# Optimization experiments

Hardware: AMD Instinct MI355X
Metric: run time of the kernel (lower is better)

The kernel has to match this reference:

```python
import jax, jax.numpy as jnp
import numpy as np

B, T, R = 32, 200, 8192
TOPK_RATIO = 0.05
K = int(R * TOPK_RATIO)            # 409 selected regions
K2 = int(R * TOPK_RATIO ** 2)      # 20 compressed features
REST = R - K                        # 7783 == rest_limitation
BN_EPS = 1e-5
NORM_EPS = 1e-12


def _linear_params(key, fan_in, fan_out):
    kw, kb = jax.random.split(key)
    bound = 1.0 / np.sqrt(fan_in)
    w = jax.random.uniform(kw, (fan_out, fan_in), jnp.float32, -bound, bound)
    b = jax.random.uniform(kb, (fan_out,), jnp.float32, -bound, bound)
    return w, b


def setup_inputs() -> dict:
    key = jax.random.key(0)
    ks = jax.random.split(key, 8)
    x = jax.random.normal(ks[0], (B, T, R), jnp.float32)
    w_proj, b_proj = _linear_params(ks[1], T, 1)
    w_process, b_process = _linear_params(ks[2], K, K)
    w_compress, b_compress = _linear_params(ks[3], K, K2)
    w_unzip, b_unzip = _linear_params(ks[4], K2, K)
    w_unprocess, b_unprocess = _linear_params(ks[5], K, K)
    w_rest, b_rest = _linear_params(ks[6], K, REST)
    bn_gamma = jnp.ones((T,), jnp.float32)
    bn_beta = jnp.zeros((T,), jnp.float32)
    return {
        "x": x,
        "w_proj": w_proj[0], "b_proj": b_proj,
        "w_process": w_process, "b_process": b_process,
        "bn_gamma": bn_gamma, "bn_beta": bn_beta,
        "w_compress": w_compress, "b_compress": b_compress,
        "w_unzip": w_unzip, "b_unzip": b_unzip,
        "w_unprocess": w_unprocess, "b_unprocess": b_unprocess,
        "w_rest": w_rest, "b_rest": b_rest,
    }


def reference(x, w_proj, b_proj, w_process, b_process, bn_gamma, bn_beta,
              w_compress, b_compress, w_unzip, b_unzip,
              w_unprocess, b_unprocess, w_rest, b_rest):
    # ---------------- Encoder ----------------
    border_mask = jnp.isnan(x)                       # [B,T,R]
    x = jnp.where(border_mask, 0.0, x)
    # F.normalize over the time axis (dim=1)
    nrm = jnp.sqrt(jnp.sum(x * x, axis=1, keepdims=True))
    x = x / jnp.maximum(nrm, NORM_EPS)
    # projection: Linear(T,1) on x.transpose(-1,-2) -> score [B,R]
    score = jnp.einsum('btr,t->br', x, w_proj) + b_proj
    border_limit = jnp.mean(border_mask.astype(x.dtype), axis=1)   # [B,R]
    score = jnp.where(border_limit.astype(bool), -10000.0, score)
    _, index = jax.lax.top_k(score, K)               # [B,K] (descending score order)
    x_topk = jnp.take_along_axis(x, index[:, None, :], axis=2)  # [B,T,K]
    sel = jnp.zeros((B, R), x.dtype).at[jnp.arange(B)[:, None], index].set(1.0)
    mask = jnp.broadcast_to(sel[:, None, :], (B, T, R))
    # process: Linear(K,K) + BatchNorm1d(T) in training mode (batch stats)
    h = jnp.einsum('btk,jk->btj', x_topk, w_process) + b_process
    mu = jnp.mean(h, axis=(0, 2), keepdims=True)
    var = jnp.var(h, axis=(0, 2), keepdims=True)     # biased, as torch BN
    h = (h - mu) / jnp.sqrt(var + BN_EPS)
    h = h * bn_gamma[None, :, None] + bn_beta[None, :, None]
    x_compress = jnp.einsum('btk,jk->btj', h, w_compress) + b_compress  # [B,T,K2]

    # ---------------- Decoder ----------------
    z = jnp.einsum('btc,kc->btk', x_compress, w_unzip) + b_unzip
    z = jnp.einsum('btk,jk->btj', z, w_unprocess) + b_unprocess          # [B,T,K]
    z_rest = jnp.einsum('btk,rk->btr', z, w_rest) + b_rest               # [B,T,REST]
    # rest positions: columns neither NaN-bordered nor topk-selected, ascending
    occupied = jnp.logical_or(sel.astype(bool), jnp.any(border_mask, axis=1))  # [B,R]
    rest_pos = jax.vmap(lambda s: jnp.argsort(s)[:REST])(occupied)       # [B,REST]

    def scat(zv, zr, idx, rp):
        xr = jnp.zeros((T, R), zv.dtype)
        xr = xr.at[:, idx].set(zv)
        xr = xr.at[:, rp].set(zr)
        return xr

    x_recon = jax.vmap(scat)(z, z_rest, index, rest_pos)                 # [B,T,R]
    return (x_recon, x_compress, mask, border_mask, index)
```

## Files before the change

kernel.cpp:

```cpp
#include <hip/hip_runtime.h>

#define Bz 32
#define Tz 200
#define Rz 8192
#define Kz 409
#define KP 416
#define K2 20
#define K2P 32
#define RESTz 7783

typedef __bf16 bf16x8 __attribute__((ext_vector_type(8)));
typedef float f32x4 __attribute__((ext_vector_type(4)));

__launch_bounds__(256)
__global__ void k_padcast(const float* __restrict__ src, __bf16* __restrict__ dst,
                          int N, int Kd, int Npad, int Kpad) {
    int i = blockIdx.x * 256 + threadIdx.x;
    int total = Npad * Kpad;
    if (i >= total) return;
    int r = i / Kpad, c = i - r * Kpad;
    float v = (r < N && c < Kd) ? src[(size_t)r * Kd + c] : 0.f;
    dst[i] = (__bf16)v;
}

__launch_bounds__(256)
__global__ void k_stats(const float* __restrict__ x, const float* __restrict__ w_proj,
                        const float* __restrict__ b_proj,
                        float* __restrict__ invnrm, float* __restrict__ score,
                        int* __restrict__ bordany, float* __restrict__ border_out) {
    const int b = blockIdx.y;
    const int c = blockIdx.x * 256 + threadIdx.x;
    const float* xp = x + (size_t)b * Tz * Rz + c;
    float* bp = border_out + (size_t)b * Tz * Rz + c;
    float p[32];
#pragma unroll
    for (int y = 0; y < 32; ++y) p[y] = 0.f;
    int nn = 0;
    for (int k = 0; k < 7; ++k) {
        const int tbase = k * 32;
#pragma unroll
        for (int y = 0; y < 32; ++y) {
            const int t = tbase + y;
            if (t < Tz) {
                float v = xp[(size_t)t * Rz];
                bool isn = (v != v);
                nn |= isn ? 1 : 0;
                float val = isn ? 0.f : v;
                bp[(size_t)t * Rz] = isn ? 1.0f : 0.0f;
                p[y] = __fadd_rn(p[y], __fmul_rn(val, val));
            }
        }
    }
#pragma unroll
    for (int off = 16; off > 0; off >>= 1)
#pragma unroll
        for (int y = 0; y < 16; ++y)
            if (y < off) p[y] = __fadd_rn(p[y], p[y + off]);
    const float ss = p[0];
    const float nv = fmaxf(__fsqrt_rn(ss), 1e-12f);
    float q[32];
#pragma unroll
    for (int y = 0; y < 32; ++y) q[y] = 0.f;
    for (int k = 0; k < 7; ++k) {
        const int tbase = k * 32;
#pragma unroll
        for (int y = 0; y < 32; ++y) {
            const int t = tbase + y;
            if (t < Tz) {
                float v = xp[(size_t)t * Rz];
                float val = (v != v) ? 0.f : v;
                float xn = __fdiv_rn(val, nv);
                float e = __fmul_rn(xn, w_proj[t]);
                q[y] = __fadd_rn(q[y], e);
            }
        }
    }
#pragma unroll
    for (int off = 16; off > 0; off >>= 1)
#pragma unroll
        for (int y = 0; y < 16; ++y)
            if (y < off) q[y] = __fadd_rn(q[y], q[y + off]);
    float sc = __fadd_rn(q[0], b_proj[0]);
    if (nn) sc = -10000.f;
    invnrm[(size_t)b * Rz + c] = __fdiv_rn(1.0f, nv);
    score[(size_t)b * Rz + c] = sc;
    bordany[(size_t)b * Rz + c] = nn;
}

__launch_bounds__(1024)
__global__ void k_topk(const float* __restrict__ score, const int* __restrict__ bordany,
                       int* __restrict__ index_ws, int* __restrict__ rest_pos,
                       float* __restrict__ o_index) {
    const int b = blockIdx.x;
    const int tid = threadIdx.x;
    __shared__ unsigned su[Rz];
    __shared__ unsigned hist[256];
    __shared__ unsigned sfx[256];
    __shared__ unsigned ckey[512];
    __shared__ unsigned cidx[512];
    __shared__ unsigned cnum;
    __shared__ unsigned sh_prefix;
    __shared__ int sh_need;
    __shared__ int scnt[1024];

    for (int i = tid; i < Rz; i += 1024) {
        unsigned u = __float_as_uint(score[(size_t)b * Rz + i]);
        u = (u & 0x80000000u) ? ~u : (u | 0x80000000u);
        su[i] = u;
    }
    __syncthreads();

    unsigned prefix = 0u, pmask = 0u;
    int need = Kz;
    for (int byte = 3; byte >= 0; --byte) {
        const int sh = byte * 8;
        if (tid < 256) hist[tid] = 0u;
        __syncthreads();
        for (int i = tid; i < Rz; i += 1024) {
            unsigned u = su[i];
            if ((u & pmask) == prefix) atomicAdd(&hist[(u >> sh) & 255u], 1u);
        }
        __syncthreads();
        if (tid < 256) sfx[tid] = hist[tid];
        __syncthreads();
        for (int off = 1; off < 256; off <<= 1) {
            unsigned add = 0u;
            if (tid < 256 && tid + off < 256) add = sfx[tid + off];
            __syncthreads();
            if (tid < 256) sfx[tid] += add;
            __syncthreads();
        }
        if (tid < 256) {
            unsigned above = (tid == 255) ? 0u : sfx[tid + 1];
            if (sfx[tid] >= (unsigned)need && above < (unsigned)need) {
                sh_need = need - (int)above;
                sh_prefix = prefix | ((unsigned)tid << sh);
            }
        }
        __syncthreads();
        prefix = sh_prefix;
        need = sh_need;
        pmask |= (0xFFu << sh);
        __syncthreads();
    }
    const unsigned Tval = prefix;

    if (tid == 0) cnum = 0u;
    __syncthreads();
    for (int i = tid; i < Rz; i += 1024) {
        unsigned u = su[i];
        if (u >= Tval) {
            unsigned p = atomicAdd(&cnum, 1u);
            if (p < 512u) { ckey[p] = u; cidx[p] = (unsigned)i; }
        }
    }
    __syncthreads();
    const int cn = (cnum < 512u) ? (int)cnum : 512;
    for (int i = tid; i < 512; i += 1024)
        if (i >= cn) { ckey[i] = 0u; cidx[i] = 0xFFFFFFFFu; }
    __syncthreads();

    for (int kk = 2; kk <= 512; kk <<= 1) {
        for (int j = kk >> 1; j > 0; j >>= 1) {
            if (tid < 256) {
                const int i = ((tid & ~(j - 1)) << 1) | (tid & (j - 1));
                const int l = i | j;
                unsigned ka = ckey[i], kb = ckey[l];
                unsigned ia = cidx[i], ib = cidx[l];
                bool a_after_b = (ka < kb) || (ka == kb && ia > ib);
                bool b_after_a = (kb < ka) || (kb == ka && ib > ia);
                bool desc = ((i & kk) == 0);
                bool dosw = desc ? a_after_b : b_after_a;
                if (dosw) { ckey[i] = kb; ckey[l] = ka; cidx[i] = ib; cidx[l] = ia; }
            }
            __syncthreads();
        }
    }

    for (int i = tid; i < Kz; i += 1024) {
        int idx = (int)(cidx[i] & 8191u);
        index_ws[b * Kz + i] = idx;
        o_index[(size_t)b * Kz + i] = (float)idx;
    }
    __syncthreads();
    for (int i = tid; i < Rz; i += 1024)
        su[i] = (bordany[(size_t)b * Rz + i] != 0) ? 1u : 0u;
    __syncthreads();
    for (int i = tid; i < Kz; i += 1024) su[cidx[i] & 8191u] = 1u;
    __syncthreads();
    int cnt = 0;
    {
        const int base = tid * 8;
#pragma unroll
        for (int o = 0; o < 8; ++o) cnt += (su[base + o] == 0u) ? 1 : 0;
    }
    scnt[tid] = cnt;
    __syncthreads();
    for (int offp = 1; offp < 1024; offp <<= 1) {
        int add = (tid >= offp) ? scnt[tid - offp] : 0;
        __syncthreads();
        scnt[tid] += add;
        __syncthreads();
    }
    const int total_un = scnt[1023];
    int run = scnt[tid] - cnt;
    const int base = tid * 8;
    for (int o = 0; o < 8; ++o) {
        const int c = base + o;
        const bool un = (su[c] == 0u);
        int pos = un ? run : (total_un + (c - run));
        if (un) run++;
        if (pos < RESTz) rest_pos[b * RESTz + pos] = c;
    }
}

__launch_bounds__(256)
__global__ void k_gather(const float* __restrict__ x, const float* __restrict__ invnrm,
                         const int* __restrict__ index_ws, __bf16* __restrict__ x_topk) {
    const int m = blockIdx.x;
    const int b = m / Tz;
    const float* xrow = x + (size_t)m * Rz;
    for (int kk = threadIdx.x; kk < KP; kk += 256) {
        float val = 0.f;
        if (kk < Kz) {
            const unsigned idx = (unsigned)index_ws[b * Kz + kk] & 8191u;
            float v = xrow[idx];
            if (v != v) v = 0.f;
            val = __fmul_rn(v, invnrm[(size_t)b * Rz + idx]);
        }
        x_topk[(size_t)m * KP + kk] = (__bf16)val;
    }
}

__launch_bounds__(256)
__global__ void k_bn(const __bf16* __restrict__ h, const float* __restrict__ gamma,
                     const float* __restrict__ beta, __bf16* __restrict__ hbn) {
    const int t = blockIdx.x;
    const int tid = threadIdx.x;
    float s = 0.f, s2 = 0.f;
    for (int i = tid; i < Bz * Kz; i += 256) {
        int b = i / Kz, j = i - b * Kz;
        float v = (float)h[(size_t)(b * Tz + t) * KP + j];
        s += v;
        s2 += v * v;
    }
    for (int off = 32; off > 0; off >>= 1) {
        s += __shfl_down(s, off);
        s2 += __shfl_down(s2, off);
    }
    __shared__ float rs[4], rs2[4];
    __shared__ float sc_sh, sf_sh;
    const int wid = tid >> 6;
    if ((tid & 63) == 0) { rs[wid] = s; rs2[wid] = s2; }
    __syncthreads();
    if (tid == 0) {
        float S = rs[0] + rs[1] + rs[2] + rs[3];
        float S2 = rs2[0] + rs2[1] + rs2[2] + rs2[3];
        const float invN = 1.f / (float)(Bz * Kz);
        float mu = S * invN;
        float var = S2 * invN - mu * mu;
        float rstd = rsqrtf(var + 1e-5f);
        float scl = gamma[t] * rstd;
        sc_sh = scl;
        sf_sh = beta[t] - mu * scl;
    }
    __syncthreads();
    const float scl = sc_sh, sft = sf_sh;
    for (int i = tid; i < Bz * KP; i += 256) {
        int b = i / KP, j = i - b * KP;
        float outv = 0.f;
        if (j < Kz) {
            float v = (float)h[(size_t)(b * Tz + t) * KP + j];
            outv = v * scl + sft;
        }
        hbn[(size_t)(b * Tz + t) * KP + j] = (__bf16)outv;
    }
}

__launch_bounds__(256)
__global__ void k_mask(const int* __restrict__ index_ws, float* __restrict__ o_mask) {
    const int bt = blockIdx.x;
    const int b = bt / Tz;
    const int tid = threadIdx.x;
    __shared__ unsigned bm[256];
    bm[tid] = 0u;
    __syncthreads();
    for (int i = tid; i < Kz; i += 256) {
        unsigned idx = (unsigned)index_ws[b * Kz + i] & 8191u;
        atomicOr(&bm[idx >> 5], 1u << (idx & 31u));
    }
    __syncthreads();
    const unsigned bits = bm[tid];
    float* dst = o_mask + (size_t)bt * Rz + tid * 32;
#pragma unroll
    for (int g = 0; g < 8; ++g) {
        float4 v;
        v.x = ((bits >> (g * 4 + 0)) & 1u) ? 1.0f : 0.0f;
        v.y = ((bits >> (g * 4 + 1)) & 1u) ? 1.0f : 0.0f;
        v.z = ((bits >> (g * 4 + 2)) & 1u) ? 1.0f : 0.0f;
        v.w = ((bits >> (g * 4 + 3)) & 1u) ? 1.0f : 0.0f;
        *(float4*)(dst + g * 4) = v;
    }
}

template <int EPI>
__launch_bounds__(256)
__global__ void k_gemm(const __bf16* __restrict__ A, int lda, int ksteps,
                       const __bf16* __restrict__ Wb, int ldb,
                       const float* __restrict__ bias,
                       __bf16* __restrict__ b_out,
                       float* __restrict__ o_xc,
                       const int* __restrict__ index_ws,
                       const int* __restrict__ rest_pos,
                       float* __restrict__ o_recon) {
    __shared__ __bf16 As[128][32];
    __shared__ __bf16 Bs[128][32];
    const int m0 = blockIdx.x * 128;
    const int n0 = blockIdx.y * 128;
    const int tid = threadIdx.x;
    const int lane = tid & 63;
    const int wid = tid >> 6;
    const int wm = wid >> 1, wn = wid & 1;
    const int r0 = lane >> 2;
    const int sg = (lane & 3) * 8;
    const int fr = lane & 15;
    const int fg = lane >> 4;
    f32x4 acc[4][4];
#pragma unroll
    for (int i = 0; i < 4; ++i)
#pragma unroll
        for (int j = 0; j < 4; ++j) {
            f32x4 z = {0.f, 0.f, 0.f, 0.f};
            acc[i][j] = z;
        }

    const int ca = wid * 16 + r0;
    const int cb = (wid + 4) * 16 + r0;
    const __bf16* gA0 = A + (size_t)(m0 + ca) * lda + sg;
    const __bf16* gA1 = A + (size_t)(m0 + cb) * lda + sg;
    const __bf16* gB0 = Wb + (size_t)(n0 + ca) * ldb + sg;
    const __bf16* gB1 = Wb + (size_t)(n0 + cb) * ldb + sg;
    __bf16* lA0 = &As[wid * 16][0];
    __bf16* lA1 = &As[(wid + 4) * 16][0];
    __bf16* lB0 = &Bs[wid * 16][0];
    __bf16* lB1 = &Bs[(wid + 4) * 16][0];

    for (int s = 0; s < ksteps; ++s) {
        const int k0 = s * 32;
        __syncthreads();
        __builtin_amdgcn_global_load_lds(gA0 + k0, lA0, 16, 0, 0);
        __builtin_amdgcn_global_load_lds(gA1 + k0, lA1, 16, 0, 0);
        __builtin_amdgcn_global_load_lds(gB0 + k0, lB0, 16, 0, 0);
        __builtin_amdgcn_global_load_lds(gB1 + k0, lB1, 16, 0, 0);
        __syncthreads();
        bf16x8 af[4], bf[4];
#pragma unroll
        for (int mi = 0; mi < 4; ++mi)
            af[mi] = *(const bf16x8*)&As[wm * 64 + mi * 16 + fr][fg * 8];
#pragma unroll
        for (int ni = 0; ni < 4; ++ni)
            bf[ni] = *(const bf16x8*)&Bs[wn * 64 + ni * 16 + fr][fg * 8];
#pragma unroll
        for (int mi = 0; mi < 4; ++mi)
#pragma unroll
            for (int ni = 0; ni < 4; ++ni)
                acc[mi][ni] = __builtin_amdgcn_mfma_f32_16x16x32_bf16(af[mi], bf[ni],
                                                                      acc[mi][ni], 0, 0, 0);
    }

#pragma unroll
    for (int mi = 0; mi < 4; ++mi)
#pragma unroll
        for (int ni = 0; ni < 4; ++ni)
#pragma unroll
            for (int rr = 0; rr < 4; ++rr) {
                const int gm = m0 + wm * 64 + mi * 16 + fg * 4 + rr;
                const int gn = n0 + wn * 64 + ni * 16 + fr;
                const float v = acc[mi][ni][rr];
                if constexpr (EPI == 0) {
                    if (gn < KP) {
                        float val = (gn < Kz) ? (v + bias[gn]) : 0.f;
                        b_out[(size_t)gm * KP + gn] = (__bf16)val;
                    }
                } else if constexpr (EPI == 1) {
                    if (gn < K2P) {
                        float val = (gn < K2) ? (v + bias[gn]) : 0.f;
                        if (gn < K2) o_xc[(size_t)gm * K2 + gn] = val;
                        b_out[(size_t)gm * K2P + gn] = (__bf16)val;
                    }
                } else if constexpr (EPI == 2) {
                    if (gn < KP) {
                        float val = (gn < Kz) ? (v + bias[gn]) : 0.f;
                        b_out[(size_t)gm * KP + gn] = (__bf16)val;
                    }
                } else if constexpr (EPI == 3) {
                    if (gn < KP) {
                        float val = (gn < Kz) ? (v + bias[gn]) : 0.f;
                        b_out[(size_t)gm * KP + gn] = (__bf16)val;
                        if (gn < Kz) {
                            const int bb = gm / Tz;
                            const unsigned col = (unsigned)index_ws[bb * Kz + gn] & 8191u;
                            o_recon[(size_t)gm * Rz + col] = val;
                        }
                    }
                } else {
                    if (gn < RESTz) {
                        const float val = v + bias[gn];
                        const int bb = gm / Tz;
                        const unsigned col = (unsigned)rest_pos[bb * RESTz + gn] & 8191u;
                        o_recon[(size_t)gm * Rz + col] = val;
                    }
                }
            }
}

extern "C" void kernel_launch(void* const* d_in, const int* in_sizes, int n_in,
                              void* d_out, int out_size, void* d_ws, size_t ws_size,
                              hipStream_t stream) {
    (void)in_sizes; (void)n_in; (void)out_size;
    const float* x           = (const float*)d_in[0];
    const float* w_proj      = (const float*)d_in[1];
    const float* b_proj      = (const float*)d_in[2];
    const float* w_process   = (const float*)d_in[3];
    const float* b_process   = (const float*)d_in[4];
    const float* bn_gamma    = (const float*)d_in[5];
    const float* bn_beta     = (const float*)d_in[6];
    const float* w_compress  = (const float*)d_in[7];
    const float* b_compress  = (const float*)d_in[8];
    const float* w_unzip     = (const float*)d_in[9];
    const float* b_unzip     = (const float*)d_in[10];
    const float* w_unprocess = (const float*)d_in[11];
    const float* b_unprocess = (const float*)d_in[12];
    const float* w_rest      = (const float*)d_in[13];
    const float* b_rest      = (const float*)d_in[14];

    float* out = (float*)d_out;
    float* o_recon  = out;
    float* o_xc     = o_recon + (size_t)Bz * Tz * Rz;
    float* o_mask   = o_xc + (size_t)Bz * Tz * K2;
    float* o_border = o_mask + (size_t)Bz * Tz * Rz;
    float* o_index  = o_border + (size_t)Bz * Tz * Rz;

    const size_t SLOT = ((size_t)Bz * Tz * KP * 2 + 255) & ~(size_t)255;
    const size_t IDXB = ((size_t)Bz * Kz * 4 + 255) & ~(size_t)255;
    const size_t RESB = ((size_t)Bz * RESTz * 4 + 255) & ~(size_t)255;
    const size_t WPB  = ((size_t)512 * KP * 2 + 255) & ~(size_t)255;
    const size_t WZB  = ((size_t)512 * K2P * 2 + 255) & ~(size_t)255;
    const size_t WCB  = ((size_t)128 * KP * 2 + 255) & ~(size_t)255;
    const size_t need = 3 * SLOT + IDXB + RESB + 2 * WPB + WZB + WCB;
    if (ws_size < need) return;

    char* ws = (char*)d_ws;
    __bf16* S1 = (__bf16*)(ws);
    __bf16* S2 = (__bf16*)(ws + SLOT);
    __bf16* S3 = (__bf16*)(ws + 2 * SLOT);
    int* index_ws = (int*)(ws + 3 * SLOT);
    int* rest_pos = (int*)(ws + 3 * SLOT + IDXB);
    __bf16* wp_b  = (__bf16*)(ws + 3 * SLOT + IDXB + RESB);
    __bf16* wup_b = (__bf16*)(ws + 3 * SLOT + IDXB + RESB + WPB);
    __bf16* wz_b  = (__bf16*)(ws + 3 * SLOT + IDXB + RESB + 2 * WPB);
    __bf16* wc_b  = (__bf16*)(ws + 3 * SLOT + IDXB + RESB + 2 * WPB + WZB);
    __bf16* wrest_b = (__bf16*)(ws);

    float* invnrm = (float*)S2;
    float* score  = invnrm + (size_t)Bz * Rz;
    int*   bordany = (int*)(score + (size_t)Bz * Rz);

    __bf16* x_topk = S1;
    __bf16* hbuf   = S2;
    __bf16* hbn    = S3;
    __bf16* xc_pad = S2;
    __bf16* z1     = S1;
    __bf16* zb     = S3;

    auto PC = [&](const float* src, __bf16* dst, int N, int Kd, int Npad, int Kpad) {
        int total = Npad * Kpad;
        k_padcast<<<dim3((total + 255) / 256), dim3(256), 0, stream>>>(src, dst, N, Kd, Npad, Kpad);
    };
    PC(w_process, wp_b, Kz, Kz, 512, KP);
    PC(w_unprocess, wup_b, Kz, Kz, 512, KP);
    PC(w_unzip, wz_b, Kz, K2, 512, K2P);
    PC(w_compress, wc_b, K2, Kz, 128, KP);

    k_stats<<<dim3(Rz / 256, Bz), dim3(256), 0, stream>>>(x, w_proj, b_proj, invnrm, score,
                                                          bordany, o_border);
    k_topk<<<dim3(Bz), dim3(1024), 0, stream>>>(score, bordany, index_ws, rest_pos, o_index);
    k_gather<<<dim3(Bz * Tz), dim3(256), 0, stream>>>(x, invnrm, index_ws, x_topk);

    dim3 blk(256);
    k_gemm<0><<<dim3(50, 4), blk, 0, stream>>>(x_topk, KP, 13, wp_b, KP, b_process,
                                               hbuf, nullptr, nullptr, nullptr, nullptr);
    k_bn<<<dim3(Tz), blk, 0, stream>>>(hbuf, bn_gamma, bn_beta, hbn);
    k_gemm<1><<<dim3(50, 1), blk, 0, stream>>>(hbn, KP, 13, wc_b, KP, b_compress,
                                               xc_pad, o_xc, nullptr, nullptr, nullptr);
    k_gemm<2><<<dim3(50, 4), blk, 0, stream>>>(xc_pad, K2P, 1, wz_b, K2P, b_unzip,
                                               z1, nullptr, nullptr, nullptr, nullptr);
    k_gemm<3><<<dim3(50, 4), blk, 0, stream>>>(z1, KP, 13, wup_b, KP, b_unprocess,
                                               zb, nullptr, index_ws, nullptr, o_recon);
    PC(w_rest, wrest_b, RESTz, Kz, 7808, KP);
    k_gemm<4><<<dim3(50, 61), blk, 0, stream>>>(zb, KP, 13, wrest_b, KP, b_rest,
                                                nullptr, nullptr, nullptr, rest_pos, o_recon);
    k_mask<<<dim3(Bz * Tz), dim3(256), 0, stream>>>(index_ws, o_mask);
}
```

Before: 604.7 us.

## Fold decoder linear chain into composed weights applied to compressed features

```diff
diff --git a/kernel.cpp b/kernel.cpp
--- a/kernel.cpp
+++ b/kernel.cpp
@@ -21,6 +21,52 @@
     int r = i / Kpad, c = i - r * Kpad;
     float v = (r < N && c < Kd) ? src[(size_t)r * Kd + c] : 0.f;
     dst[i] = (__bf16)v;
+}
+
+__launch_bounds__(32)
+__global__ void k_wu(const float* __restrict__ wup, const float* __restrict__ wz,
+                     const float* __restrict__ b_uz, const float* __restrict__ b_up,
+                     float* __restrict__ WU_f, float* __restrict__ bU,
+                     __bf16* __restrict__ WU_b) {
+    const int i = blockIdx.x;
+    const int c = threadIdx.x;
+    if (i >= Kz) {
+        if (c < K2P) WU_b[(size_t)i * K2P + c] = (__bf16)0.f;
+        return;
+    }
+    const float* row = wup + (size_t)i * Kz;
+    float acc = 0.f;
+    if (c < K2) {
+        for (int j = 0; j < Kz; ++j) acc = fmaf(row[j], wz[(size_t)j * K2 + c], acc);
+        WU_f[(size_t)i * K2 + c] = acc;
+        WU_b[(size_t)i * K2P + c] = (__bf16)acc;
+    } else if (c == K2) {
+        for (int j = 0; j < Kz; ++j) acc = fmaf(row[j], b_uz[j], acc);
+        bU[i] = acc + b_up[i];
+    }
+    if (c >= K2 && c < K2P) WU_b[(size_t)i * K2P + c] = (__bf16)0.f;
+}
+
+__launch_bounds__(32)
+__global__ void k_wr(const float* __restrict__ wr, const float* __restrict__ b_r,
+                     const float* __restrict__ WU_f, const float* __restrict__ bU,
+                     __bf16* __restrict__ WR_b, float* __restrict__ bR) {
+    const int r = blockIdx.x;
+    const int c = threadIdx.x;
+    if (r >= RESTz) {
+        if (c < K2P) WR_b[(size_t)r * K2P + c] = (__bf16)0.f;
+        return;
+    }
+    const float* row = wr + (size_t)r * Kz;
+    float acc = 0.f;
+    if (c < K2) {
+        for (int i = 0; i < Kz; ++i) acc = fmaf(row[i], WU_f[(size_t)i * K2 + c], acc);
+        WR_b[(size_t)r * K2P + c] = (__bf16)acc;
+    } else if (c == K2) {
+        for (int i = 0; i < Kz; ++i) acc = fmaf(row[i], bU[i], acc);
+        bR[r] = acc + b_r[r];
+    }
+    if (c >= K2 && c < K2P) WR_b[(size_t)r * K2P + c] = (__bf16)0.f;
 }
 
 __launch_bounds__(256)
@@ -388,20 +434,12 @@
                         if (gn < K2) o_xc[(size_t)gm * K2 + gn] = val;
                         b_out[(size_t)gm * K2P + gn] = (__bf16)val;
                     }
-                } else if constexpr (EPI == 2) {
-                    if (gn < KP) {
-                        float val = (gn < Kz) ? (v + bias[gn]) : 0.f;
-                        b_out[(size_t)gm * KP + gn] = (__bf16)val;
-                    }
                 } else if constexpr (EPI == 3) {
-                    if (gn < KP) {
-                        float val = (gn < Kz) ? (v + bias[gn]) : 0.f;
-                        b_out[(size_t)gm * KP + gn] = (__bf16)val;
-                        if (gn < Kz) {
-                            const int bb = gm / Tz;
-                            const unsigned col = (unsigned)index_ws[bb * Kz + gn] & 8191u;
-                            o_recon[(size_t)gm * Rz + col] = val;
-                        }
+                    if (gn < Kz) {
+                        float val = v + bias[gn];
+                        const int bb = gm / Tz;
+                        const unsigned col = (unsigned)index_ws[bb * Kz + gn] & 8191u;
+                        o_recon[(size_t)gm * Rz + col] = val;
                     }
                 } else {
                     if (gn < RESTz) {
@@ -445,22 +483,30 @@
     const size_t IDXB = ((size_t)Bz * Kz * 4 + 255) & ~(size_t)255;
     const size_t RESB = ((size_t)Bz * RESTz * 4 + 255) & ~(size_t)255;
     const size_t WPB  = ((size_t)512 * KP * 2 + 255) & ~(size_t)255;
-    const size_t WZB  = ((size_t)512 * K2P * 2 + 255) & ~(size_t)255;
     const size_t WCB  = ((size_t)128 * KP * 2 + 255) & ~(size_t)255;
-    const size_t need = 3 * SLOT + IDXB + RESB + 2 * WPB + WZB + WCB;
+    const size_t WUF  = ((size_t)Kz * K2 * 4 + 255) & ~(size_t)255;
+    const size_t BUB  = ((size_t)512 * 4 + 255) & ~(size_t)255;
+    const size_t WUB  = ((size_t)512 * K2P * 2 + 255) & ~(size_t)255;
+    const size_t WRB  = ((size_t)7808 * K2P * 2 + 255) & ~(size_t)255;
+    const size_t BRB  = ((size_t)7808 * 4 + 255) & ~(size_t)255;
+    const size_t need = 3 * SLOT + IDXB + RESB + WPB + WCB + WUF + BUB + WUB + WRB + BRB;
     if (ws_size < need) return;
 
     char* ws = (char*)d_ws;
-    __bf16* S1 = (__bf16*)(ws);
-    __bf16* S2 = (__bf16*)(ws + SLOT);
-    __bf16* S3 = (__bf16*)(ws + 2 * SLOT);
-    int* index_ws = (int*)(ws + 3 * SLOT);
-    int* rest_pos = (int*)(ws + 3 * SLOT + IDXB);
-    __bf16* wp_b  = (__bf16*)(ws + 3 * SLOT + IDXB + RESB);
-    __bf16* wup_b = (__bf16*)(ws + 3 * SLOT + IDXB + RESB + WPB);
-    __bf16* wz_b  = (__bf16*)(ws + 3 * SLOT + IDXB + RESB + 2 * WPB);
-    __bf16* wc_b  = (__bf16*)(ws + 3 * SLOT + IDXB + RESB + 2 * WPB + WZB);
-    __bf16* wrest_b = (__bf16*)(ws);
+    size_t off = 0;
+    auto AL = [&](size_t n) { void* p = ws + off; off += n; return p; };
+    __bf16* S1 = (__bf16*)AL(SLOT);
+    __bf16* S2 = (__bf16*)AL(SLOT);
+    __bf16* S3 = (__bf16*)AL(SLOT);
+    int* index_ws = (int*)AL(IDXB);
+    int* rest_pos = (int*)AL(RESB);
+    __bf16* wp_b  = (__bf16*)AL(WPB);
+    __bf16* wc_b  = (__bf16*)AL(WCB);
+    float*  WU_f  = (float*)AL(WUF);
+    float*  bU    = (float*)AL(BUB);
+    __bf16* WU_b  = (__bf16*)AL(WUB);
+    __bf16* WR_b  = (__bf16*)AL(WRB);
+    float*  bR    = (float*)AL(BRB);
 
     float* invnrm = (float*)S2;
     float* score  = invnrm + (size_t)Bz * Rz;
@@ -470,17 +516,17 @@
     __bf16* hbuf   = S2;
     __bf16* hbn    = S3;
     __bf16* xc_pad = S2;
-    __bf16* z1     = S1;
-    __bf16* zb     = S3;
+    __bf16* zb     = S1;
 
     auto PC = [&](const float* src, __bf16* dst, int N, int Kd, int Npad, int Kpad) {
         int total = Npad * Kpad;
         k_padcast<<<dim3((total + 255) / 256), dim3(256), 0, stream>>>(src, dst, N, Kd, Npad, Kpad);
     };
     PC(w_process, wp_b, Kz, Kz, 512, KP);
-    PC(w_unprocess, wup_b, Kz, Kz, 512, KP);
-    PC(w_unzip, wz_b, Kz, K2, 512, K2P);
     PC(w_compress, wc_b, K2, Kz, 128, KP);
+    k_wu<<<dim3(512), dim3(32), 0, stream>>>(w_unprocess, w_unzip, b_unzip, b_unprocess,
+                                             WU_f, bU, WU_b);
+    k_wr<<<dim3(7808), dim3(32), 0, stream>>>(w_rest, b_rest, WU_f, bU, WR_b, bR);
 
     k_stats<<<dim3(Rz / 256, Bz), dim3(256), 0, stream>>>(x, w_proj, b_proj, invnrm, score,
                                                           bordany, o_border);
@@ -493,12 +539,9 @@
     k_bn<<<dim3(Tz), blk, 0, stream>>>(hbuf, bn_gamma, bn_beta, hbn);
     k_gemm<1><<<dim3(50, 1), blk, 0, stream>>>(hbn, KP, 13, wc_b, KP, b_compress,
                                                xc_pad, o_xc, nullptr, nullptr, nullptr);
-    k_gemm<2><<<dim3(50, 4), blk, 0, stream>>>(xc_pad, K2P, 1, wz_b, K2P, b_unzip,
-                                               z1, nullptr, nullptr, nullptr, nullptr);
-    k_gemm<3><<<dim3(50, 4), blk, 0, stream>>>(z1, KP, 13, wup_b, KP, b_unprocess,
+    k_gemm<3><<<dim3(50, 4), blk, 0, stream>>>(xc_pad, K2P, 1, WU_b, K2P, bU,
                                                zb, nullptr, index_ws, nullptr, o_recon);
-    PC(w_rest, wrest_b, RESTz, Kz, 7808, KP);
-    k_gemm<4><<<dim3(50, 61), blk, 0, stream>>>(zb, KP, 13, wrest_b, KP, b_rest,
+    k_gemm<4><<<dim3(50, 61), blk, 0, stream>>>(xc_pad, K2P, 1, WR_b, K2P, bR,
                                                 nullptr, nullptr, nullptr, rest_pos, o_recon);
     k_mask<<<dim3(Bz * Tz), dim3(256), 0, stream>>>(index_ws, o_mask);
 }
```

Result: slower. 687.8 us (+13.7%).
